# Kernel tuning notes

Hardware: AMD Instinct MI355X
Metric: run time of the kernel (lower is better)

The kernel has to match this reference:

```python
import jax, jax.numpy as jnp
import numpy as np

WEIGHT_FACTOR = 0.8


def _pairwise_l2(f):
    # ||a-b|| via GEMM trick: ||a||^2 + ||b||^2 - 2 a.b, avoiding the [N,N,D] blowup.
    sqn = jnp.sum(f * f, axis=1)                      # [N]
    sq = sqn[:, None] + sqn[None, :] - 2.0 * (f @ f.T)  # [N,N]
    sq = jnp.maximum(sq, 0.0)
    pos = sq > 0
    # safe sqrt: subgradient 0 at zero distance (matches torch.norm at 0)
    return jnp.where(pos, jnp.sqrt(jnp.where(pos, sq, 1.0)), 0.0)


def _mse(a, b):
    d = a - b
    return jnp.mean(d * d)


def setup_inputs() -> dict:
    key = jax.random.key(0)
    ks = jax.random.split(key, 8)
    N, D, C = 4096, 256, 1000
    return {
        "pred": jax.random.normal(ks[0], (N, C), dtype=jnp.float32),
        "target": jax.random.normal(ks[1], (N, C), dtype=jnp.float32),
        "pred_f0": jax.random.normal(ks[2], (N, D), dtype=jnp.float32),
        "pred_f1": jax.random.normal(ks[3], (N, D), dtype=jnp.float32),
        "pred_f2": jax.random.normal(ks[4], (N, D), dtype=jnp.float32),
        "target_f0": jax.random.normal(ks[5], (N, D), dtype=jnp.float32),
        "target_f1": jax.random.normal(ks[6], (N, D), dtype=jnp.float32),
        "target_f2": jax.random.normal(ks[7], (N, D), dtype=jnp.float32),
    }


def reference(pred, target, pred_f0, pred_f1, pred_f2, target_f0, target_f1, target_f2):
    pred_feats = (pred_f0, pred_f1, pred_f2)
    target_feats = (target_f0, target_f1, target_f2)
    num_features = len(pred_feats)

    label_loss = _mse(pred, target)
    feature_loss = 0.0
    for pf, tf in zip(pred_feats, target_feats):
        feature_loss = feature_loss + _mse(_pairwise_l2(pf), _pairwise_l2(tf))
    return (1.0 - WEIGHT_FACTOR) * label_loss + WEIGHT_FACTOR * feature_loss / num_features
```

## Files before the change

kernel.cpp:

```cpp
#include <hip/hip_runtime.h>
#include <stdint.h>

#define NR 4096
#define DD 256
#define NC_TOT 4096000
#define TILES 32
#define NTRI 528
#define NBLK_GRAM 256

typedef float f32x4 __attribute__((ext_vector_type(4)));
typedef unsigned char u8;

#define WS_MSEP_OFF  256
#define WS_FEATP_OFF 16384
#define WS_SQN_OFF   32768
#define WS_FP8_OFF   131072

__global__ __launch_bounds__(256) void prep_mse_kernel(
    const float* __restrict__ m0, const float* __restrict__ m1,
    const float* __restrict__ m2, const float* __restrict__ m3,
    const float* __restrict__ m4, const float* __restrict__ m5,
    const float4* __restrict__ pred, const float4* __restrict__ target,
    u8* __restrict__ q8, float* __restrict__ sqn, float* __restrict__ msep,
    unsigned* __restrict__ cnt)
{
    __shared__ float sr[4];
    const int t = threadIdx.x, w = t >> 6, lane = t & 63;
    const int y = blockIdx.y;
    if (y == 0 && blockIdx.x == 0 && t == 0) *cnt = 0u;

    if (y < 6) {
        const float* mp = m0;
        if (y == 1) mp = m1;
        else if (y == 2) mp = m2;
        else if (y == 3) mp = m3;
        else if (y == 4) mp = m4;
        else if (y == 5) mp = m5;
        const int R = blockIdx.x * 4 + w;
        const int P = R >> 7, rr = R & 127;
        const float4* src = (const float4*)(mp + (size_t)R * DD);
        float4 v = src[lane];
        float ss = v.x * v.x + v.y * v.y + v.z * v.z + v.w * v.w;
        unsigned lo = __builtin_amdgcn_cvt_pk_fp8_f32(v.x, v.y, 0u, false);
        unsigned hi = __builtin_amdgcn_cvt_pk_fp8_f32(v.z, v.w, 0u, false);
        unsigned packed = (lo & 0xffffu) | (hi << 16);
        size_t idx = ((size_t)(y * 32 + P) << 15)
                     + (size_t)(lane >> 1) * 1024 + rr * 8 + (lane & 1) * 4;
        *(unsigned*)(q8 + idx) = packed;
        #pragma unroll
        for (int off = 32; off; off >>= 1) ss += __shfl_down(ss, off);
        if (lane == 0) sqn[(size_t)y * NR + R] = ss;
    } else {
        const int b2 = (y - 6) * 1024 + blockIdx.x;
        float s = 0.f;
        for (int i = b2 * 256 + t; i < NC_TOT / 4; i += 2048 * 256) {
            float4 x = pred[i], yv = target[i];
            float dx = x.x - yv.x, dy = x.y - yv.y;
            float dz = x.z - yv.z, dw = x.w - yv.w;
            s += dx * dx + dy * dy + dz * dz + dw * dw;
        }
        #pragma unroll
        for (int off = 32; off; off >>= 1) s += __shfl_down(s, off);
        if (lane == 0) sr[w] = s;
        __syncthreads();
        if (t == 0) msep[b2] = sr[0] + sr[1] + sr[2] + sr[3];
    }
}

#define COMPUTE_STAGE(BI, ACC)                                                 \
  do {                                                                         \
    const u8* tA_ = &buf[BI][0];                                               \
    const u8* tB_ = &buf[BI][32768];                                           \
    _Pragma("unroll")                                                          \
    for (int kc = 0; kc < 8; kc++) {                                           \
      const int gg = kc * 4 + quad;                                            \
      long a_[4], b_[2];                                                       \
      _Pragma("unroll")                                                        \
      for (int mi = 0; mi < 4; mi++)                                           \
        a_[mi] = *(const long*)&tA_[gg * 1024 + (wm * 64 + mi * 16 + l16) * 8];\
      _Pragma("unroll")                                                        \
      for (int ni = 0; ni < 2; ni++)                                           \
        b_[ni] = *(const long*)&tB_[gg * 1024 + (wn * 32 + ni * 16 + l16) * 8];\
      _Pragma("unroll")                                                        \
      for (int mi = 0; mi < 4; mi++)                                           \
        _Pragma("unroll")                                                      \
        for (int ni = 0; ni < 2; ni++)                                         \
          ACC[mi][ni] = __builtin_amdgcn_mfma_f32_16x16x32_fp8_fp8(            \
              a_[mi], b_[ni], ACC[mi][ni], 0, 0, 0);                           \
    }                                                                          \
  } while (0)

#define RESET_ACC()                                                            \
  do {                                                                         \
    _Pragma("unroll")                                                          \
    for (int a4 = 0; a4 < 4; a4++)                                             \
      _Pragma("unroll")                                                        \
      for (int b2 = 0; b2 < 2; b2++) {                                         \
        accp[a4][b2] = f32x4{0.f, 0.f, 0.f, 0.f};                              \
        acct[a4][b2] = f32x4{0.f, 0.f, 0.f, 0.f};                              \
      }                                                                        \
  } while (0)

__global__ __launch_bounds__(512) void gram_loss_kernel(
    const u8* __restrict__ q8, const float* __restrict__ sqn,
    float* __restrict__ featp, const float* __restrict__ msep,
    unsigned* __restrict__ cnt, float* __restrict__ out)
{
    __shared__ u8 buf[2][65536];
    __shared__ float s_red[8];
    __shared__ int s_last;

    const int xcd = blockIdx.x & 7, slot = blockIdx.x >> 3;
    const int t = threadIdx.x;
    const int w = t >> 6, lane = t & 63;
    const int wm = w >> 2, wn = w & 3;
    const int quad = lane >> 4, l16 = lane & 15;
    const char* qb = (const char*)q8;

    auto tile_of = [&](int k, int& f, int& ti, int& tj) -> bool {
        int idx = slot + 32 * k, lin;
        if (xcd < 6) {
            if (idx >= 196) return false;
            f = xcd >> 1; lin = (xcd & 1) + 2 * idx;
        } else {
            if (idx >= 204) return false;
            int rr = (xcd - 6) + 2 * idx;
            f = rr / 136; lin = 392 + rr - f * 136;
        }
        int a = 0, rem = lin;
        while (rem >= TILES - a) { rem -= TILES - a; a++; }
        ti = a; tj = a + rem;
        return true;
    };

    auto prefetch = [&](int b, int f, int ti, int tj, int tgt) {
        const int m = f + 3 * tgt;
        const size_t bA = ((size_t)(m * 32 + ti)) << 15;
        const size_t bB = ((size_t)(m * 32 + tj)) << 15;
        const char* g = qb + ((w < 4) ? bA : bB) + (w & 3) * 8192 + lane * 16;
        char* l = (char*)&buf[b][0] + ((w < 4) ? 0 : 32768) + (w & 3) * 8192;
        #pragma unroll
        for (int i = 0; i < 8; i++)
            __builtin_amdgcn_global_load_lds(
                (const __attribute__((address_space(1))) void*)(g + i * 1024),
                (__attribute__((address_space(3))) void*)(l + i * 1024), 16, 0, 0);
    };

    f32x4 accp[4][2], acct[4][2];
    RESET_ACC();

    float local = 0.f;

    int fc, tic, tjc;
    tile_of(0, fc, tic, tjc);
    prefetch(0, fc, tic, tjc, 0);
    __syncthreads();

    int k = 0;
    while (true) {
        prefetch(1, fc, tic, tjc, 1);
        COMPUTE_STAGE(0, accp);
        __syncthreads();

        int fn, tin, tjn;
        const bool more = tile_of(k + 1, fn, tin, tjn);
        if (more) prefetch(0, fn, tin, tjn, 0);
        COMPUTE_STAGE(1, acct);

        {
            const float* sqp = sqn + (size_t)fc * NR;
            const float* sqt = sqn + (size_t)(3 + fc) * NR;
            const bool diag = (tic == tjc);
            float tl = 0.f;
            #pragma unroll
            for (int mi = 0; mi < 4; mi++) {
                const int i0 = wm * 64 + mi * 16 + quad * 4;
                const f32x4 sip = *(const f32x4*)(sqp + tic * 128 + i0);
                const f32x4 sit = *(const f32x4*)(sqt + tic * 128 + i0);
                #pragma unroll
                for (int ni = 0; ni < 2; ni++) {
                    const int j_loc = wn * 32 + ni * 16 + l16;
                    const float spj = sqp[tjc * 128 + j_loc];
                    const float stj = sqt[tjc * 128 + j_loc];
                    const f32x4 gp = accp[mi][ni], gt = acct[mi][ni];
                    #pragma unroll
                    for (int r = 0; r < 4; r++) {
                        float dp2 = fmaxf(fmaf(-2.f, gp[r], sip[r] + spj), 0.f);
                        float dt2 = fmaxf(fmaf(-2.f, gt[r], sit[r] + stj), 0.f);
                        if (diag && (i0 + r == j_loc)) { dp2 = 0.f; dt2 = 0.f; }
                        float sq = __builtin_amdgcn_sqrtf(dp2 * dt2);
                        tl += fmaf(-2.f, sq, dp2 + dt2);
                    }
                }
            }
            local += diag ? tl : 2.f * tl;
            RESET_ACC();
        }
        __syncthreads();
        if (!more) break;
        k++;
        fc = fn; tic = tin; tjc = tjn;
    }

    #pragma unroll
    for (int off = 32; off; off >>= 1) local += __shfl_down(local, off);
    if (lane == 0) s_red[w] = local;
    __syncthreads();
    if (t == 0) {
        float bs = 0.f;
        #pragma unroll
        for (int i = 0; i < 8; i++) bs += s_red[i];
        featp[blockIdx.x] = bs;
        __threadfence();
        unsigned old = atomicAdd(cnt, 1u);
        s_last = (old == NBLK_GRAM - 1) ? 1 : 0;
    }
    __syncthreads();

    if (s_last) {
        __threadfence();
        float s2 = 0.f, m2 = 0.f;
        for (int i = t; i < NBLK_GRAM; i += 512) s2 += featp[i];
        for (int i = t; i < 2048; i += 512) m2 += msep[i];
        #pragma unroll
        for (int off = 32; off; off >>= 1) {
            s2 += __shfl_down(s2, off);
            m2 += __shfl_down(m2, off);
        }
        __shared__ float fr[8], mr[8];
        if (lane == 0) { fr[w] = s2; mr[w] = m2; }
        __syncthreads();
        if (t == 0) {
            float fs = 0.f, ms = 0.f;
            #pragma unroll
            for (int i = 0; i < 8; i++) { fs += fr[i]; ms += mr[i]; }
            out[0] = 0.2f * (ms / (float)NC_TOT) +
                     (0.8f / 3.0f) * (fs / ((float)NR * (float)NR));
        }
    }
}

extern "C" void kernel_launch(void* const* d_in, const int* in_sizes, int n_in,
                              void* d_out, int out_size, void* d_ws, size_t ws_size,
                              hipStream_t stream) {
    unsigned* cnt  = (unsigned*)d_ws;
    float* msep    = (float*)((char*)d_ws + WS_MSEP_OFF);
    float* featp   = (float*)((char*)d_ws + WS_FEATP_OFF);
    float* sqn     = (float*)((char*)d_ws + WS_SQN_OFF);
    u8* q8         = (u8*)((char*)d_ws + WS_FP8_OFF);

    prep_mse_kernel<<<dim3(1024, 8), 256, 0, stream>>>(
        (const float*)d_in[2], (const float*)d_in[3], (const float*)d_in[4],
        (const float*)d_in[5], (const float*)d_in[6], (const float*)d_in[7],
        (const float4*)d_in[0], (const float4*)d_in[1], q8, sqn, msep, cnt);

    gram_loss_kernel<<<NBLK_GRAM, 512, 0, stream>>>(
        q8, sqn, featp, msep, cnt, (float*)d_out);
}
```

Before: 143.1 us.

## Drop LDS staging in gram kernel, fold label MSE in, double block count

The gram kernel no longer stages FP8 tiles through double-buffered LDS with global_load_lds. Each wave now loads its MFMA operand fragments straight from global memory. This frees the 128KB of shared memory, removes the block-wide syncs and allows more resident blocks (launch_bounds 512,4 and 512 blocks). The label MSE reduction moves from the prep kernel into the gram kernel's prologue, and tile assignment is rotated per slot, iteration and XCD. The trade-off is redundant global/L1 traffic, because several waves re-read the same A/B fragments, and there is no explicit prefetch overlap.

```diff
diff --git a/kernel.cpp b/kernel.cpp
--- a/kernel.cpp
+++ b/kernel.cpp
@@ -6,7 +6,7 @@
 #define NC_TOT 4096000
 #define TILES 32
 #define NTRI 528
-#define NBLK_GRAM 256
+#define NBLK_GRAM 512
 
 typedef float f32x4 __attribute__((ext_vector_type(4)));
 typedef unsigned char u8;
@@ -20,67 +20,45 @@
     const float* __restrict__ m0, const float* __restrict__ m1,
     const float* __restrict__ m2, const float* __restrict__ m3,
     const float* __restrict__ m4, const float* __restrict__ m5,
-    const float4* __restrict__ pred, const float4* __restrict__ target,
-    u8* __restrict__ q8, float* __restrict__ sqn, float* __restrict__ msep,
-    unsigned* __restrict__ cnt)
+    u8* __restrict__ q8, float* __restrict__ sqn, unsigned* __restrict__ cnt)
 {
-    __shared__ float sr[4];
     const int t = threadIdx.x, w = t >> 6, lane = t & 63;
     const int y = blockIdx.y;
     if (y == 0 && blockIdx.x == 0 && t == 0) *cnt = 0u;
 
-    if (y < 6) {
-        const float* mp = m0;
-        if (y == 1) mp = m1;
-        else if (y == 2) mp = m2;
-        else if (y == 3) mp = m3;
-        else if (y == 4) mp = m4;
-        else if (y == 5) mp = m5;
-        const int R = blockIdx.x * 4 + w;
-        const int P = R >> 7, rr = R & 127;
-        const float4* src = (const float4*)(mp + (size_t)R * DD);
-        float4 v = src[lane];
-        float ss = v.x * v.x + v.y * v.y + v.z * v.z + v.w * v.w;
-        unsigned lo = __builtin_amdgcn_cvt_pk_fp8_f32(v.x, v.y, 0u, false);
-        unsigned hi = __builtin_amdgcn_cvt_pk_fp8_f32(v.z, v.w, 0u, false);
-        unsigned packed = (lo & 0xffffu) | (hi << 16);
-        size_t idx = ((size_t)(y * 32 + P) << 15)
-                     + (size_t)(lane >> 1) * 1024 + rr * 8 + (lane & 1) * 4;
-        *(unsigned*)(q8 + idx) = packed;
-        #pragma unroll
-        for (int off = 32; off; off >>= 1) ss += __shfl_down(ss, off);
-        if (lane == 0) sqn[(size_t)y * NR + R] = ss;
-    } else {
-        const int b2 = (y - 6) * 1024 + blockIdx.x;
-        float s = 0.f;
-        for (int i = b2 * 256 + t; i < NC_TOT / 4; i += 2048 * 256) {
-            float4 x = pred[i], yv = target[i];
-            float dx = x.x - yv.x, dy = x.y - yv.y;
-            float dz = x.z - yv.z, dw = x.w - yv.w;
-            s += dx * dx + dy * dy + dz * dz + dw * dw;
-        }
-        #pragma unroll
-        for (int off = 32; off; off >>= 1) s += __shfl_down(s, off);
-        if (lane == 0) sr[w] = s;
-        __syncthreads();
-        if (t == 0) msep[b2] = sr[0] + sr[1] + sr[2] + sr[3];
-    }
+    const float* mp = m0;
+    if (y == 1) mp = m1;
+    else if (y == 2) mp = m2;
+    else if (y == 3) mp = m3;
+    else if (y == 4) mp = m4;
+    else if (y == 5) mp = m5;
+    const int R = blockIdx.x * 4 + w;
+    const int P = R >> 7, rr = R & 127;
+    const float4* src = (const float4*)(mp + (size_t)R * DD);
+    float4 v = src[lane];
+    float ss = v.x * v.x + v.y * v.y + v.z * v.z + v.w * v.w;
+    unsigned lo = __builtin_amdgcn_cvt_pk_fp8_f32(v.x, v.y, 0u, false);
+    unsigned hi = __builtin_amdgcn_cvt_pk_fp8_f32(v.z, v.w, 0u, false);
+    unsigned packed = (lo & 0xffffu) | (hi << 16);
+    size_t idx = ((size_t)(y * 32 + P) << 15)
+                 + (size_t)(lane >> 1) * 1024 + rr * 8 + (lane & 1) * 4;
+    *(unsigned*)(q8 + idx) = packed;
+    #pragma unroll
+    for (int off = 32; off; off >>= 1) ss += __shfl_down(ss, off);
+    if (lane == 0) sqn[(size_t)y * NR + R] = ss;
 }
 
-#define COMPUTE_STAGE(BI, ACC)                                                 \
+#define COMPUTE_DIRECT(PA, PB, ACC)                                            \
   do {                                                                         \
-    const u8* tA_ = &buf[BI][0];                                               \
-    const u8* tB_ = &buf[BI][32768];                                           \
     _Pragma("unroll")                                                          \
     for (int kc = 0; kc < 8; kc++) {                                           \
-      const int gg = kc * 4 + quad;                                            \
       long a_[4], b_[2];                                                       \
       _Pragma("unroll")                                                        \
       for (int mi = 0; mi < 4; mi++)                                           \
-        a_[mi] = *(const long*)&tA_[gg * 1024 + (wm * 64 + mi * 16 + l16) * 8];\
+        a_[mi] = *(const long*)((PA) + kc * 4096 + aoff + mi * 128);           \
       _Pragma("unroll")                                                        \
       for (int ni = 0; ni < 2; ni++)                                           \
-        b_[ni] = *(const long*)&tB_[gg * 1024 + (wn * 32 + ni * 16 + l16) * 8];\
+        b_[ni] = *(const long*)((PB) + kc * 4096 + boff + ni * 128);           \
       _Pragma("unroll")                                                        \
       for (int mi = 0; mi < 4; mi++)                                           \
         _Pragma("unroll")                                                      \
@@ -101,13 +79,13 @@
       }                                                                        \
   } while (0)
 
-__global__ __launch_bounds__(512) void gram_loss_kernel(
+__global__ __launch_bounds__(512, 4) void gram_loss_kernel(
     const u8* __restrict__ q8, const float* __restrict__ sqn,
-    float* __restrict__ featp, const float* __restrict__ msep,
+    const float4* __restrict__ pred, const float4* __restrict__ target,
+    float* __restrict__ featp, float* __restrict__ msep,
     unsigned* __restrict__ cnt, float* __restrict__ out)
 {
-    __shared__ u8 buf[2][65536];
-    __shared__ float s_red[8];
+    __shared__ float s_red[8], s_mse[8];
     __shared__ int s_last;
 
     const int xcd = blockIdx.x & 7, slot = blockIdx.x >> 3;
@@ -117,8 +95,20 @@
     const int quad = lane >> 4, l16 = lane & 15;
     const char* qb = (const char*)q8;
 
+    const int aoff = quad * 1024 + (wm * 64 + l16) * 8;
+    const int boff = quad * 1024 + (wn * 32 + l16) * 8;
+
+    float mse = 0.f;
+    for (int i = blockIdx.x * 512 + t; i < NC_TOT / 4; i += NBLK_GRAM * 512) {
+        float4 x = pred[i], yv = target[i];
+        float dx = x.x - yv.x, dy = x.y - yv.y;
+        float dz = x.z - yv.z, dw = x.w - yv.w;
+        mse += dx * dx + dy * dy + dz * dz + dw * dw;
+    }
+
     auto tile_of = [&](int k, int& f, int& ti, int& tj) -> bool {
-        int idx = slot + 32 * k, lin;
+        int rs = (slot + k * 21 + xcd * 9) & 63;
+        int idx = rs + (k << 6), lin;
         if (xcd < 6) {
             if (idx >= 196) return false;
             f = xcd >> 1; lin = (xcd & 1) + 2 * idx;
@@ -133,39 +123,22 @@
         return true;
     };
 
-    auto prefetch = [&](int b, int f, int ti, int tj, int tgt) {
-        const int m = f + 3 * tgt;
-        const size_t bA = ((size_t)(m * 32 + ti)) << 15;
-        const size_t bB = ((size_t)(m * 32 + tj)) << 15;
-        const char* g = qb + ((w < 4) ? bA : bB) + (w & 3) * 8192 + lane * 16;
-        char* l = (char*)&buf[b][0] + ((w < 4) ? 0 : 32768) + (w & 3) * 8192;
-        #pragma unroll
-        for (int i = 0; i < 8; i++)
-            __builtin_amdgcn_global_load_lds(
-                (const __attribute__((address_space(1))) void*)(g + i * 1024),
-                (__attribute__((address_space(3))) void*)(l + i * 1024), 16, 0, 0);
-    };
-
     f32x4 accp[4][2], acct[4][2];
     RESET_ACC();
 
     float local = 0.f;
 
     int fc, tic, tjc;
-    tile_of(0, fc, tic, tjc);
-    prefetch(0, fc, tic, tjc, 0);
-    __syncthreads();
-
     int k = 0;
-    while (true) {
-        prefetch(1, fc, tic, tjc, 1);
-        COMPUTE_STAGE(0, accp);
-        __syncthreads();
-
-        int fn, tin, tjn;
-        const bool more = tile_of(k + 1, fn, tin, tjn);
-        if (more) prefetch(0, fn, tin, tjn, 0);
-        COMPUTE_STAGE(1, acct);
+    bool more = tile_of(0, fc, tic, tjc);
+    while (more) {
+        const char* pA = qb + (((size_t)(fc * 32 + tic)) << 15);
+        const char* pB = qb + (((size_t)(fc * 32 + tjc)) << 15);
+        const char* tA = qb + (((size_t)((3 + fc) * 32 + tic)) << 15);
+        const char* tB = qb + (((size_t)((3 + fc) * 32 + tjc)) << 15);
+
+        COMPUTE_DIRECT(pA, pB, accp);
+        COMPUTE_DIRECT(tA, tB, acct);
 
         {
             const float* sqp = sqn + (size_t)fc * NR;
@@ -196,21 +169,23 @@
             local += diag ? tl : 2.f * tl;
             RESET_ACC();
         }
-        __syncthreads();
-        if (!more) break;
         k++;
-        fc = fn; tic = tin; tjc = tjn;
+        more = tile_of(k, fc, tic, tjc);
     }
 
     #pragma unroll
-    for (int off = 32; off; off >>= 1) local += __shfl_down(local, off);
-    if (lane == 0) s_red[w] = local;
+    for (int off = 32; off; off >>= 1) {
+        local += __shfl_down(local, off);
+        mse   += __shfl_down(mse, off);
+    }
+    if (lane == 0) { s_red[w] = local; s_mse[w] = mse; }
     __syncthreads();
     if (t == 0) {
-        float bs = 0.f;
+        float bs = 0.f, ms = 0.f;
         #pragma unroll
-        for (int i = 0; i < 8; i++) bs += s_red[i];
+        for (int i = 0; i < 8; i++) { bs += s_red[i]; ms += s_mse[i]; }
         featp[blockIdx.x] = bs;
+        msep[blockIdx.x]  = ms;
         __threadfence();
         unsigned old = atomicAdd(cnt, 1u);
         s_last = (old == NBLK_GRAM - 1) ? 1 : 0;
@@ -220,8 +195,10 @@
     if (s_last) {
         __threadfence();
         float s2 = 0.f, m2 = 0.f;
-        for (int i = t; i < NBLK_GRAM; i += 512) s2 += featp[i];
-        for (int i = t; i < 2048; i += 512) m2 += msep[i];
+        for (int i = t; i < NBLK_GRAM; i += 512) {
+            s2 += featp[i];
+            m2 += msep[i];
+        }
         #pragma unroll
         for (int off = 32; off; off >>= 1) {
             s2 += __shfl_down(s2, off);
@@ -249,11 +226,12 @@
     float* sqn     = (float*)((char*)d_ws + WS_SQN_OFF);
     u8* q8         = (u8*)((char*)d_ws + WS_FP8_OFF);
 
-    prep_mse_kernel<<<dim3(1024, 8), 256, 0, stream>>>(
+    prep_mse_kernel<<<dim3(1024, 6), 256, 0, stream>>>(
         (const float*)d_in[2], (const float*)d_in[3], (const float*)d_in[4],
         (const float*)d_in[5], (const float*)d_in[6], (const float*)d_in[7],
-        (const float4*)d_in[0], (const float4*)d_in[1], q8, sqn, msep, cnt);
+        q8, sqn, cnt);
 
     gram_loss_kernel<<<NBLK_GRAM, 512, 0, stream>>>(
-        q8, sqn, featp, msep, cnt, (float*)d_out);
+        q8, sqn, (const float4*)d_in[0], (const float4*)d_in[1],
+        featp, msep, cnt, (float*)d_out);
 }
```

Measured after the change: 156.8 us. 9.5% more time.
